# Optimization experiments

Measured on AMD Instinct MI355X. Metric: run time of the kernel, lower is better.

The kernel has to match this reference:

```python
import jax, jax.numpy as jnp
import numpy as np

VOCAB, EMBED, HIDDEN, CH = 500, 80, 512, 128
B, L, T = 128, 784, 256


def setup_inputs() -> dict:
    key = jax.random.key(0)
    ks = jax.random.split(key, 14)
    s = lambda fan_in: 1.0 / np.sqrt(fan_in)
    return {
        "latent_rep": jax.random.normal(ks[0], (B, L, CH), jnp.float32),
        "formulas": jax.random.randint(ks[1], (B, T), 0, VOCAB),
        "embedding": jax.random.normal(ks[2], (VOCAB, EMBED), jnp.float32),
        "W_ih": jax.random.uniform(ks[3], (4 * HIDDEN, HIDDEN + EMBED), jnp.float32, -s(HIDDEN), s(HIDDEN)),
        "b_ih": jax.random.uniform(ks[4], (4 * HIDDEN,), jnp.float32, -s(HIDDEN), s(HIDDEN)),
        "W_hh": jax.random.uniform(ks[5], (4 * HIDDEN, HIDDEN), jnp.float32, -s(HIDDEN), s(HIDDEN)),
        "b_hh": jax.random.uniform(ks[6], (4 * HIDDEN,), jnp.float32, -s(HIDDEN), s(HIDDEN)),
        "Wh": jax.random.uniform(ks[7], (HIDDEN, CH), jnp.float32, -s(CH), s(CH)),
        "bh": jax.random.uniform(ks[8], (HIDDEN,), jnp.float32, -s(CH), s(CH)),
        "Wc": jax.random.uniform(ks[9], (HIDDEN, CH), jnp.float32, -s(CH), s(CH)),
        "bc": jax.random.uniform(ks[10], (HIDDEN,), jnp.float32, -s(CH), s(CH)),
        "Wo": jax.random.uniform(ks[11], (HIDDEN, CH), jnp.float32, -s(CH), s(CH)),
        "bo": jax.random.uniform(ks[12], (HIDDEN,), jnp.float32, -s(CH), s(CH)),
    }


def reference(latent_rep, formulas, embedding, W_ih, b_ih, W_hh, b_hh, Wh, bh, Wc, bc, Wo, bo):
    # init_lstm: tanh(Linear(mean over spatial positions))
    mean_lr = latent_rep.mean(axis=1)                       # [B, C]
    h0 = jnp.tanh(mean_lr @ Wh.T + bh)                       # [B, H]
    c0 = jnp.tanh(mean_lr @ Wc.T + bc)
    o0 = jnp.tanh(mean_lr @ Wo.T + bo)                       # fixed across steps in source

    emb = embedding[formulas]                                # [B, T, E]
    xs = jnp.swapaxes(emb, 0, 1)                             # [T, B, E]

    def step(carry, emb_t):
        h, c = carry
        inp = jnp.concatenate([o0, emb_t], axis=1)           # [B, H+E]
        gates = inp @ W_ih.T + b_ih + h @ W_hh.T + b_hh      # [B, 4H]
        i_g, f_g, g_g, o_g = jnp.split(gates, 4, axis=1)
        c_new = jax.nn.sigmoid(f_g) * c + jax.nn.sigmoid(i_g) * jnp.tanh(g_g)
        h_new = jax.nn.sigmoid(o_g) * jnp.tanh(c_new)
        # dropout in eval mode = identity
        return (h_new, c_new), h_new

    _, hs = jax.lax.scan(step, (h0, c0), xs)                 # hs: [T, B, H]
    return jnp.swapaxes(hs, 0, 1)                            # [B, T, H]
```

## Files before the change

kernel.cpp:

```cpp
#include <hip/hip_runtime.h>
#include <hip/hip_bf16.h>
#include <stdint.h>

typedef unsigned int uint32;
typedef __attribute__((ext_vector_type(8))) short short8;
typedef __attribute__((ext_vector_type(4))) float f32x4;

#define NB 128
#define NT 256
#define NH 512
#define NE 80
#define NCH 128
#define NL 784
#define NV 500
#define NG4 2048

__device__ __forceinline__ unsigned short f2bf(float f){
  union { float f; unsigned int i; } v; v.f = f;
  unsigned int r = v.i + 0x7FFFu + ((v.i >> 16) & 1u);
  return (unsigned short)(r >> 16);
}
__device__ __forceinline__ float sigf(float x){ return 1.0f/(1.0f + __expf(-x)); }
__device__ __forceinline__ float tanhfast(float x){ return 1.0f - 2.0f/(__expf(2.0f*x)+1.0f); }

__global__ void k_mean(const float* __restrict__ lat, float* __restrict__ meanv){
  int b = blockIdx.x;
  int tid = threadIdx.x;
  int c4 = tid & 31;
  int part = tid >> 5;
  const float4* row = (const float4*)(lat + (size_t)b*NL*NCH);
  float sx=0.f, sy=0.f, sz=0.f, sw=0.f;
  for (int l=part; l<NL; l+=8){
    float4 v = row[l*32 + c4];
    sx+=v.x; sy+=v.y; sz+=v.z; sw+=v.w;
  }
  __shared__ float red[8][32][4];
  red[part][c4][0]=sx; red[part][c4][1]=sy; red[part][c4][2]=sz; red[part][c4][3]=sw;
  __syncthreads();
  if (part==0){
    float a0=0,a1=0,a2=0,a3=0;
    #pragma unroll
    for (int p=0;p<8;p++){ a0+=red[p][c4][0]; a1+=red[p][c4][1]; a2+=red[p][c4][2]; a3+=red[p][c4][3]; }
    float4 o; o.x=a0*(1.0f/NL); o.y=a1*(1.0f/NL); o.z=a2*(1.0f/NL); o.w=a3*(1.0f/NL);
    ((float4*)meanv)[b*32 + c4] = o;
  }
}

__global__ void k_init(const float* __restrict__ meanv,
    const float* __restrict__ Wh, const float* __restrict__ bh,
    const float* __restrict__ Wc, const float* __restrict__ bc,
    const float* __restrict__ Wo, const float* __restrict__ bo,
    float* __restrict__ c0, float* __restrict__ o0, unsigned short* __restrict__ hbuf0){
  int b = blockIdx.x; int j = threadIdx.x;
  const float* m = meanv + b*NCH;
  const float4* wh = (const float4*)(Wh + (size_t)j*NCH);
  const float4* wc = (const float4*)(Wc + (size_t)j*NCH);
  const float4* wo = (const float4*)(Wo + (size_t)j*NCH);
  float sh=0.f, sc=0.f, so=0.f;
  for (int c=0; c<NCH/4; c++){
    float4 vh = wh[c], vc = wc[c], vo = wo[c];
    float m0=m[c*4], m1=m[c*4+1], m2=m[c*4+2], m3=m[c*4+3];
    sh += m0*vh.x + m1*vh.y + m2*vh.z + m3*vh.w;
    sc += m0*vc.x + m1*vc.y + m2*vc.z + m3*vc.w;
    so += m0*vo.x + m1*vo.y + m2*vo.z + m3*vo.w;
  }
  float h0 = tanhf(sh + bh[j]);
  c0[b*NH+j] = tanhf(sc + bc[j]);
  o0[b*NH+j] = tanhf(so + bo[j]);
  hbuf0[b*NH+j] = f2bf(h0);
}

__global__ void k_table(const float* __restrict__ emb,
                        const float* __restrict__ Wih,
                        float* __restrict__ table){
  int v = blockIdx.x;
  int n = blockIdx.y*256 + threadIdx.x;
  const float4* wr = (const float4*)(Wih + (size_t)n*(NH+NE) + NH);
  const float4* er = (const float4*)(emb + v*NE);
  float s = 0.f;
  for (int e4=0; e4<NE/4; e4++){
    float4 w = wr[e4], e = er[e4];
    s += w.x*e.x + w.y*e.y + w.z*e.z + w.w*e.w;
  }
  table[(size_t)v*NG4 + n] = s;
}

__global__ void k_base(const float* __restrict__ o0,
                       const float* __restrict__ Wih,
                       const float* __restrict__ bih,
                       const float* __restrict__ bhh,
                       float* __restrict__ base){
  int b = blockIdx.x;
  int n = blockIdx.y*256 + threadIdx.x;
  const float4* o = (const float4*)(o0 + b*NH);
  const float4* wr = (const float4*)(Wih + (size_t)n*(NH+NE));
  float s = bih[n] + bhh[n];
  for (int k4=0;k4<NH/4;k4++){
    float4 w = wr[k4], v = o[k4];
    s += w.x*v.x + w.y*v.y + w.z*v.z + w.w*v.w;
  }
  base[(size_t)b*NG4 + n] = s;
}

#define HBUF_U (NB*(NH/2))

__global__ __launch_bounds__(256, 1) void k_lstm(
    const float* __restrict__ Whh,
    const int* __restrict__ formulas,
    const float* __restrict__ table,
    const float* __restrict__ base,
    const float* __restrict__ c0,
    uint32* hbuf, int* flags,
    float* __restrict__ out)
{
  int bid = blockIdx.x;
  int g = bid & 7, s = bid >> 3;
  int tid = threadIdx.x;
  int lane = tid & 63, w = tid >> 6;
  int b0 = g*16, u0 = s*32;

  __shared__ __align__(16) char h_lds[16*1024];
  __shared__ float G[16*132 + 4];

  short8 bw[2][16];
  {
    int krow = (lane >> 4) * 8;
    #pragma unroll
    for (int h2=0; h2<2; h2++){
      int c_loc = w*32 + h2*16 + (lane & 15);
      int wrow = (c_loc >> 5)*NH + u0 + (c_loc & 31);
      const float4* p4 = (const float4*)(Whh + (size_t)wrow*NH + krow);
      #pragma unroll
      for (int ks=0; ks<16; ks++){
        float4 lo = p4[ks*8], hi = p4[ks*8+1];
        short8 t;
        t[0]=(short)f2bf(lo.x); t[1]=(short)f2bf(lo.y); t[2]=(short)f2bf(lo.z); t[3]=(short)f2bf(lo.w);
        t[4]=(short)f2bf(hi.x); t[5]=(short)f2bf(hi.y); t[6]=(short)f2bf(hi.z); t[7]=(short)f2bf(hi.w);
        bw[h2][ks] = t;
      }
    }
  }

  int r_e = tid >> 4, up = tid & 15;
  int be = b0 + r_e;
  float cst0 = c0[be*NH + u0 + 2*up];
  float cst1 = c0[be*NH + u0 + 2*up + 1];

  float2 bsv[4];
  #pragma unroll
  for (int gt=0; gt<4; gt++)
    bsv[gt] = *(const float2*)(base + (size_t)be*NG4 + gt*NH + u0 + 2*up);

  float2 tbv[4];
  {
    int tok0 = formulas[be*NT + 0];
    #pragma unroll
    for (int gt=0; gt<4; gt++)
      tbv[gt] = *(const float2*)(table + (size_t)tok0*NG4 + gt*NH + u0 + 2*up);
  }

  int arow = lane & 15;
  int abyte = arow*1024 + ((lane>>4)*8)*2;
  int aswz = (arow & 7) << 4;

  int* myflag = flags + g*16 + s;
  const int* pollptr = flags + g*16 + (lane & 15);

  for (int t=0; t<NT; t++){
    const uint32* hrd = hbuf + (t & 1)*HBUF_U;
    uint32*       hwr = hbuf + ((t+1) & 1)*HBUF_U;

    if (t > 0){
      if (w == 0){
        int guard = 0;
        while (1){
          int v = __hip_atomic_load(pollptr, __ATOMIC_RELAXED, __HIP_MEMORY_SCOPE_AGENT);
          if (__all(v >= t)) break;
          __builtin_amdgcn_s_sleep(1);
          if (++guard > (1<<16)) break;
        }
      }
      __syncthreads();
    }

    uint32 vals[16];
    #pragma unroll
    for (int it=0; it<16; it++){
      int i = tid + it*256;
      int r = i >> 8, cu = i & 255;
      vals[it] = __hip_atomic_load(&hrd[(b0+r)*(NH/2) + cu],
                                   __ATOMIC_RELAXED, __HIP_MEMORY_SCOPE_AGENT);
    }
    #pragma unroll
    for (int it=0; it<16; it++){
      int i = tid + it*256;
      int r = i >> 8, cu = i & 255;
      *(uint32*)(h_lds + ((r*1024 + cu*4) ^ ((r & 7) << 4))) = vals[it];
    }
    __syncthreads();

    f32x4 acc0 = {0.f,0.f,0.f,0.f}, acc1 = {0.f,0.f,0.f,0.f};
    #pragma unroll
    for (int ks=0; ks<16; ks++){
      short8 a = *(const short8*)(h_lds + ((abyte + ks*64) ^ aswz));
      acc0 = __builtin_amdgcn_mfma_f32_16x16x32_bf16(a, bw[0][ks], acc0, 0, 0, 0);
      acc1 = __builtin_amdgcn_mfma_f32_16x16x32_bf16(a, bw[1][ks], acc1, 0, 0, 0);
    }

    {
      int rbase = (lane>>4)*4;
      int col0 = (w*2+0)*16 + (lane&15);
      int col1 = (w*2+1)*16 + (lane&15);
      #pragma unroll
      for (int r4=0;r4<4;r4++){
        G[(rbase+r4)*132 + col0] = acc0[r4];
        G[(rbase+r4)*132 + col1] = acc1[r4];
      }
    }
    __syncthreads();

    float hn0, hn1;
    {
      const float* Gr = G + r_e*132 + 2*up;
      float gi0 = Gr[0]   + tbv[0].x + bsv[0].x;
      float gi1 = Gr[1]   + tbv[0].y + bsv[0].y;
      float gf0 = Gr[32]  + tbv[1].x + bsv[1].x;
      float gf1 = Gr[33]  + tbv[1].y + bsv[1].y;
      float gg0 = Gr[64]  + tbv[2].x + bsv[2].x;
      float gg1 = Gr[65]  + tbv[2].y + bsv[2].y;
      float go0 = Gr[96]  + tbv[3].x + bsv[3].x;
      float go1 = Gr[97]  + tbv[3].y + bsv[3].y;
      float cn0 = sigf(gf0)*cst0 + sigf(gi0)*tanhfast(gg0);
      float cn1 = sigf(gf1)*cst1 + sigf(gi1)*tanhfast(gg1);
      cst0 = cn0; cst1 = cn1;
      hn0 = sigf(go0)*tanhfast(cn0);
      hn1 = sigf(go1)*tanhfast(cn1);
    }

    if (t < NT-1){
      uint32 packed = (uint32)f2bf(hn0) | ((uint32)f2bf(hn1) << 16);
      __hip_atomic_store(&hwr[be*(NH/2) + (u0/2 + up)], packed,
                         __ATOMIC_RELAXED, __HIP_MEMORY_SCOPE_AGENT);
    }
    __syncthreads();
    if (t < NT-1 && tid == 0)
      __hip_atomic_store(myflag, t+1, __ATOMIC_RELAXED, __HIP_MEMORY_SCOPE_AGENT);

    {
      float2 ov; ov.x = hn0; ov.y = hn1;
      *(float2*)(out + ((size_t)be*NT + t)*NH + u0 + 2*up) = ov;
    }
    if (t < NT-1){
      int tokn = formulas[be*NT + t + 1];
      #pragma unroll
      for (int gt=0; gt<4; gt++)
        tbv[gt] = *(const float2*)(table + (size_t)tokn*NG4 + gt*NH + u0 + 2*up);
    }
  }
}

extern "C" void kernel_launch(void* const* d_in, const int* in_sizes, int n_in,
                              void* d_out, int out_size, void* d_ws, size_t ws_size,
                              hipStream_t stream) {
  const float* lat      = (const float*)d_in[0];
  const int*   formulas = (const int*)d_in[1];
  const float* emb      = (const float*)d_in[2];
  const float* Wih      = (const float*)d_in[3];
  const float* bih      = (const float*)d_in[4];
  const float* Whh      = (const float*)d_in[5];
  const float* bhh      = (const float*)d_in[6];
  const float* Wh       = (const float*)d_in[7];
  const float* bh       = (const float*)d_in[8];
  const float* Wc       = (const float*)d_in[9];
  const float* bc       = (const float*)d_in[10];
  const float* Wo       = (const float*)d_in[11];
  const float* bo       = (const float*)d_in[12];
  float* out = (float*)d_out;

  char* ws = (char*)d_ws;
  float* meanv = (float*)ws;  ws += (size_t)NB*NCH*4;
  float* c0    = (float*)ws;  ws += (size_t)NB*NH*4;
  float* o0    = (float*)ws;  ws += (size_t)NB*NH*4;
  float* table = (float*)ws;  ws += (size_t)NV*NG4*4;
  float* base  = (float*)ws;  ws += (size_t)NB*NG4*4;
  uint32* hbuf = (uint32*)ws; ws += (size_t)2*HBUF_U*4;
  int*   flags = (int*)ws;    ws += 512;

  hipMemsetAsync(flags, 0, 512, stream);
  k_mean <<<NB, 256, 0, stream>>>(lat, meanv);
  k_init <<<NB, NH, 0, stream>>>(meanv, Wh, bh, Wc, bc, Wo, bo, c0, o0, (unsigned short*)hbuf);
  k_table<<<dim3(NV, 8), 256, 0, stream>>>(emb, Wih, table);
  k_base <<<dim3(NB, 8), 256, 0, stream>>>(o0, Wih, bih, bhh, base);
  k_lstm <<<NB, 256, 0, stream>>>(Whh, formulas, table, base, c0, hbuf, flags, out);
}
```

Measured before the change: 712.6 us.

## Replace per-block flag polling with epoch-tagged 64-bit hidden-state words

The cross-block handoff of the hidden state between recurrent steps now packs each bf16 pair with a 32-bit step tag into one 64-bit atomic word. Readers spin on the data itself until every tag matches the current step, so the separate flag array, flag polling loop, and the extra block barrier plus flag store after each step are removed. This cuts one round trip of global synchronisation per timestep but doubles the bytes read and written for the hidden state. Readers may also spin on many words instead of one flag.

```diff
diff --git a/kernel.cpp b/kernel.cpp
--- a/kernel.cpp
+++ b/kernel.cpp
@@ -3,6 +3,7 @@
 #include <stdint.h>
 
 typedef unsigned int uint32;
+typedef unsigned long long uint64;
 typedef __attribute__((ext_vector_type(8))) short short8;
 typedef __attribute__((ext_vector_type(4))) float f32x4;
 
@@ -14,6 +15,8 @@
 #define NL 784
 #define NV 500
 #define NG4 2048
+
+#define HB_PAIRS (NB*(NH/2))
 
 __device__ __forceinline__ unsigned short f2bf(float f){
   union { float f; unsigned int i; } v; v.f = f;
@@ -50,8 +53,9 @@
     const float* __restrict__ Wh, const float* __restrict__ bh,
     const float* __restrict__ Wc, const float* __restrict__ bc,
     const float* __restrict__ Wo, const float* __restrict__ bo,
-    float* __restrict__ c0, float* __restrict__ o0, unsigned short* __restrict__ hbuf0){
+    float* __restrict__ c0, float* __restrict__ o0, uint64* __restrict__ hbuf){
   int b = blockIdx.x; int j = threadIdx.x;
+  __shared__ unsigned short hsh[NH];
   const float* m = meanv + b*NCH;
   const float4* wh = (const float4*)(Wh + (size_t)j*NCH);
   const float4* wc = (const float4*)(Wc + (size_t)j*NCH);
@@ -67,7 +71,12 @@
   float h0 = tanhf(sh + bh[j]);
   c0[b*NH+j] = tanhf(sc + bc[j]);
   o0[b*NH+j] = tanhf(so + bo[j]);
-  hbuf0[b*NH+j] = f2bf(h0);
+  hsh[j] = f2bf(h0);
+  __syncthreads();
+  if (j < NH/2){
+    uint32 packed = (uint32)hsh[2*j] | ((uint32)hsh[2*j+1] << 16);
+    hbuf[(size_t)b*(NH/2) + j] = (uint64)packed;
+  }
 }
 
 __global__ void k_table(const float* __restrict__ emb,
@@ -102,15 +111,13 @@
   base[(size_t)b*NG4 + n] = s;
 }
 
-#define HBUF_U (NB*(NH/2))
-
 __global__ __launch_bounds__(256, 1) void k_lstm(
     const float* __restrict__ Whh,
     const int* __restrict__ formulas,
     const float* __restrict__ table,
     const float* __restrict__ base,
     const float* __restrict__ c0,
-    uint32* hbuf, int* flags,
+    uint64* hbuf,
     float* __restrict__ out)
 {
   int bid = blockIdx.x;
@@ -163,39 +170,35 @@
   int abyte = arow*1024 + ((lane>>4)*8)*2;
   int aswz = (arow & 7) << 4;
 
-  int* myflag = flags + g*16 + s;
-  const int* pollptr = flags + g*16 + (lane & 15);
-
   for (int t=0; t<NT; t++){
-    const uint32* hrd = hbuf + (t & 1)*HBUF_U;
-    uint32*       hwr = hbuf + ((t+1) & 1)*HBUF_U;
-
-    if (t > 0){
-      if (w == 0){
-        int guard = 0;
-        while (1){
-          int v = __hip_atomic_load(pollptr, __ATOMIC_RELAXED, __HIP_MEMORY_SCOPE_AGENT);
-          if (__all(v >= t)) break;
-          __builtin_amdgcn_s_sleep(1);
-          if (++guard > (1<<16)) break;
-        }
-      }
-      __syncthreads();
-    }
-
-    uint32 vals[16];
-    #pragma unroll
-    for (int it=0; it<16; it++){
-      int i = tid + it*256;
-      int r = i >> 8, cu = i & 255;
-      vals[it] = __hip_atomic_load(&hrd[(b0+r)*(NH/2) + cu],
-                                   __ATOMIC_RELAXED, __HIP_MEMORY_SCOPE_AGENT);
-    }
-    #pragma unroll
-    for (int it=0; it<16; it++){
-      int i = tid + it*256;
-      int r = i >> 8, cu = i & 255;
-      *(uint32*)(h_lds + ((r*1024 + cu*4) ^ ((r & 7) << 4))) = vals[it];
+    uint64* hrd = hbuf + (size_t)(t & 1)*HB_PAIRS;
+    uint64* hwr = hbuf + (size_t)((t+1) & 1)*HB_PAIRS;
+    const uint32 etag = (uint32)t;
+
+    uint64 vv[16];
+    #pragma unroll
+    for (int i=0;i<16;i++)
+      vv[i] = __hip_atomic_load(&hrd[(size_t)b0*(NH/2) + tid + i*256],
+                                __ATOMIC_RELAXED, __HIP_MEMORY_SCOPE_AGENT);
+    uint32 stale = 0;
+    #pragma unroll
+    for (int i=0;i<16;i++) if ((uint32)(vv[i] >> 32) != etag) stale |= 1u << i;
+    int guard = 0;
+    while (stale && ++guard < (1<<16)){
+      #pragma unroll
+      for (int i=0;i<16;i++) if (stale & (1u << i))
+        vv[i] = __hip_atomic_load(&hrd[(size_t)b0*(NH/2) + tid + i*256],
+                                  __ATOMIC_RELAXED, __HIP_MEMORY_SCOPE_AGENT);
+      stale = 0;
+      #pragma unroll
+      for (int i=0;i<16;i++) if ((uint32)(vv[i] >> 32) != etag) stale |= 1u << i;
+    }
+
+    #pragma unroll
+    for (int i=0;i<16;i++){
+      int p = tid + i*256;
+      int r = p >> 8, cu = p & 255;
+      *(uint32*)(h_lds + ((r*1024 + cu*4) ^ ((r & 7) << 4))) = (uint32)vv[i];
     }
     __syncthreads();
 
@@ -239,12 +242,10 @@
 
     if (t < NT-1){
       uint32 packed = (uint32)f2bf(hn0) | ((uint32)f2bf(hn1) << 16);
-      __hip_atomic_store(&hwr[be*(NH/2) + (u0/2 + up)], packed,
+      uint64 pv = (uint64)packed | ((uint64)(uint32)(t+1) << 32);
+      __hip_atomic_store(&hwr[(size_t)be*(NH/2) + (u0/2 + up)], pv,
                          __ATOMIC_RELAXED, __HIP_MEMORY_SCOPE_AGENT);
     }
-    __syncthreads();
-    if (t < NT-1 && tid == 0)
-      __hip_atomic_store(myflag, t+1, __ATOMIC_RELAXED, __HIP_MEMORY_SCOPE_AGENT);
 
     {
       float2 ov; ov.x = hn0; ov.y = hn1;
@@ -283,13 +284,12 @@
   float* o0    = (float*)ws;  ws += (size_t)NB*NH*4;
   float* table = (float*)ws;  ws += (size_t)NV*NG4*4;
   float* base  = (float*)ws;  ws += (size_t)NB*NG4*4;
-  uint32* hbuf = (uint32*)ws; ws += (size_t)2*HBUF_U*4;
-  int*   flags = (int*)ws;    ws += 512;
-
-  hipMemsetAsync(flags, 0, 512, stream);
+  uint64* hbuf = (uint64*)ws; ws += (size_t)2*HB_PAIRS*8;
+
+  hipMemsetAsync(hbuf, 0, (size_t)2*HB_PAIRS*8, stream);
   k_mean <<<NB, 256, 0, stream>>>(lat, meanv);
-  k_init <<<NB, NH, 0, stream>>>(meanv, Wh, bh, Wc, bc, Wo, bo, c0, o0, (unsigned short*)hbuf);
+  k_init <<<NB, NH, 0, stream>>>(meanv, Wh, bh, Wc, bc, Wo, bo, c0, o0, hbuf);
   k_table<<<dim3(NV, 8), 256, 0, stream>>>(emb, Wih, table);
   k_base <<<dim3(NB, 8), 256, 0, stream>>>(o0, Wih, bih, bhh, base);
-  k_lstm <<<NB, 256, 0, stream>>>(Whh, formulas, table, base, c0, hbuf, flags, out);
-}
+  k_lstm <<<NB, 256, 0, stream>>>(Whh, formulas, table, base, c0, hbuf, out);
+}
```

Result: slower. 740.7 us (+3.9%).
